# Optimization experiments

Hardware: AMD Instinct MI355X
Metric: run time of the kernel (lower is better)

## Reference

```python
import jax, jax.numpy as jnp
import numpy as np

B, S, D, H = 16, 512, 1024, 16
DH = D // H  # 64


def setup_inputs() -> dict:
    key = jax.random.key(0)
    kx, kq, kk, kv = jax.random.split(key, 4)
    stdv = 1.0 / np.sqrt(DH)  # reset_param uses 1/sqrt(t.size(1)) = 1/sqrt(head_dim)
    x = jax.random.normal(kx, (B, S, D), dtype=jnp.float32)
    Wq = jax.random.uniform(kq, (H, D, DH), dtype=jnp.float32, minval=-stdv, maxval=stdv)
    Wk = jax.random.uniform(kk, (H, D, DH), dtype=jnp.float32, minval=-stdv, maxval=stdv)
    Wv = jax.random.uniform(kv, (H, D, DH), dtype=jnp.float32, minval=-stdv, maxval=stdv)
    return {"x": x, "Wq": Wq, "Wk": Wk, "Wv": Wv}


def reference(x, Wq, Wk, Wv):
    # x: [B, S, D]; Wq/Wk/Wv: [H, D, DH] (stacked per-head params)
    q = jnp.einsum('bsd,hde->bhse', x, Wq)  # [B,H,S,DH]
    k = jnp.einsum('bsd,hde->bhse', x, Wk)
    v = jnp.einsum('bsd,hde->bhse', x, Wv)
    # NOTE: original scales by sqrt(input_dim), not sqrt(head_dim)
    scale = 1.0 / jnp.sqrt(jnp.float32(D))
    scores = jnp.einsum('bhse,bhte->bhst', q, k) * scale  # [B,H,S,S]
    attn = jax.nn.softmax(scores, axis=-1)
    out = jnp.einsum('bhst,bhte->bhse', attn, v)  # [B,H,S,DH]
    # concat heads along feature dim (head order matches torch cat over loop)
    return out.transpose(0, 2, 1, 3).reshape(x.shape[0], x.shape[1], D)
```

## Files before the change

kernel.cpp:

```cpp
#include <hip/hip_runtime.h>
#include <math.h>

constexpr int B = 16, S = 512, D = 1024, H = 16, DH = 64;
constexpr int BH = B * H;

typedef short bf16x8 __attribute__((ext_vector_type(8)));
typedef float f32x4  __attribute__((ext_vector_type(4)));

__device__ __forceinline__ unsigned short f2bf(float f) {
    unsigned u = __float_as_uint(f);
    u += 0x7fff + ((u >> 16) & 1);
    return (unsigned short)(u >> 16);
}

__global__ __launch_bounds__(256) void convert_x(
    const float* __restrict__ x, unsigned short* __restrict__ xb)
{
    int i = blockIdx.x * 256 + threadIdx.x;
    float4 v = ((const float4*)x)[i];
    ushort4 o;
    o.x = f2bf(v.x); o.y = f2bf(v.y); o.z = f2bf(v.z); o.w = f2bf(v.w);
    ((ushort4*)xb)[i] = o;
}

__global__ __launch_bounds__(256) void convert_w(
    const float* __restrict__ Wq, const float* __restrict__ Wk,
    const float* __restrict__ Wv, unsigned short* __restrict__ WbT)
{
    __shared__ float tile[64][65];
    const int d0 = blockIdx.x * 64;
    const int h = blockIdx.y, m = blockIdx.z;
    const float* W = ((m == 0) ? Wq : (m == 1) ? Wk : Wv) + (size_t)h * D * DH;
    const int t = threadIdx.x;
    {
        int e = t & 63, dr = t >> 6;
        #pragma unroll
        for (int i = 0; i < 16; ++i) {
            int d = dr * 16 + i;
            tile[d][e] = W[(size_t)(d0 + d) * DH + e];
        }
    }
    __syncthreads();
    {
        int d = t & 63, er = t >> 6;
        unsigned short* out = WbT + (size_t)(m * H + h) * DH * D;
        #pragma unroll
        for (int i = 0; i < 16; ++i) {
            int e = er * 16 + i;
            out[(size_t)e * D + d0 + d] = f2bf(tile[d][e]);
        }
    }
}

__global__ __launch_bounds__(256) void qkv_gemm(
    const unsigned short* __restrict__ xb,
    const unsigned short* __restrict__ WbT,
    unsigned short* __restrict__ qkvb)
{
    __shared__ unsigned short As[128 * 64];
    __shared__ unsigned short Bs[128 * 64];

    const int t = threadIdx.x;
    const int w = t >> 6;
    const int wr = w >> 1, wc = w & 1;
    const int L = t & 63;
    const int lane15 = L & 15;
    const int quad = L >> 4;
    const int lrow8 = L >> 3;
    const int lg = L & 7;

    const int r0 = blockIdx.x * 128;
    const int n0 = blockIdx.y * 128;

    f32x4 acc[4][4] = {};

    for (int k0 = 0; k0 < D; k0 += 64) {
        #pragma unroll
        for (int i = 0; i < 4; ++i) {
            int c = w * 4 + i;
            int r = c * 8 + lrow8;
            int gg = lg ^ (r & 7);
            const unsigned short* gp = xb + (size_t)(r0 + r) * D + k0 + gg * 8;
            __builtin_amdgcn_global_load_lds(
                (const __attribute__((address_space(1))) void*)gp,
                (__attribute__((address_space(3))) void*)(As + c * 512),
                16, 0, 0);
            const unsigned short* gq = WbT + (size_t)(n0 + r) * D + k0 + gg * 8;
            __builtin_amdgcn_global_load_lds(
                (const __attribute__((address_space(1))) void*)gq,
                (__attribute__((address_space(3))) void*)(Bs + c * 512),
                16, 0, 0);
        }
        __syncthreads();

        #pragma unroll
        for (int ks = 0; ks < 2; ++ks) {
            int gk = ks * 4 + quad;
            bf16x8 a[4], bb[4];
            #pragma unroll
            for (int rt = 0; rt < 4; ++rt) {
                int ml = wr * 64 + rt * 16 + lane15;
                a[rt] = *(const bf16x8*)(As + ml * 64 + ((gk ^ (ml & 7)) * 8));
            }
            #pragma unroll
            for (int ct = 0; ct < 4; ++ct) {
                int nl = wc * 64 + ct * 16 + lane15;
                bb[ct] = *(const bf16x8*)(Bs + nl * 64 + ((gk ^ (nl & 7)) * 8));
            }
            #pragma unroll
            for (int rt = 0; rt < 4; ++rt)
                #pragma unroll
                for (int ct = 0; ct < 4; ++ct)
                    acc[rt][ct] = __builtin_amdgcn_mfma_f32_16x16x32_bf16(
                        a[rt], bb[ct], acc[rt][ct], 0, 0, 0);
        }
        __syncthreads();
    }

    const int m  = n0 >> 10;
    const int h  = ((n0 >> 6) + wc) & 15;
    const int bb_ = r0 >> 9;
    const int s0 = (r0 & 511) + wr * 64;

    if (m == 2) {
        unsigned short* outv = qkvb + ((size_t)(2 * BH) + (bb_ * H + h)) * (size_t)(S * DH);
        #pragma unroll
        for (int rt = 0; rt < 4; ++rt) {
            int srow = s0 + rt * 16 + quad * 4;
            #pragma unroll
            for (int ct = 0; ct < 4; ++ct) {
                int e = ct * 16 + lane15;
                ushort4 pk;
                pk.x = f2bf(acc[rt][ct][0]);
                pk.y = f2bf(acc[rt][ct][1]);
                pk.z = f2bf(acc[rt][ct][2]);
                pk.w = f2bf(acc[rt][ct][3]);
                *(ushort4*)(outv + (size_t)e * S + srow) = pk;
            }
        }
    } else {
        const float sc = (m == 0) ? 0.04508422002778011f : 1.0f;
        unsigned short* out = qkvb + ((size_t)m * BH + (bb_ * H + h)) * (size_t)(S * DH);
        #pragma unroll
        for (int rt = 0; rt < 4; ++rt) {
            #pragma unroll
            for (int ct = 0; ct < 4; ++ct) {
                int e = ct * 16 + lane15;
                #pragma unroll
                for (int r = 0; r < 4; ++r) {
                    int srow = s0 + rt * 16 + quad * 4 + r;
                    out[(size_t)srow * DH + e] = f2bf(acc[rt][ct][r] * sc);
                }
            }
        }
    }
}

__global__ __launch_bounds__(256) void attn_mfma(
    const unsigned short* __restrict__ qkvb, float* __restrict__ out)
{
    __shared__ unsigned short Qs[128 * 64];
    __shared__ unsigned short Ks[64 * 64];
    __shared__ unsigned short Vt[64 * 64];

    const int t = threadIdx.x;
    const int w = t >> 6;
    const int L = t & 63;
    const int lane15 = L & 15;
    const int quad = L >> 4;
    const int lrow8 = L >> 3;
    const int lg = L & 7;
    const int qr0 = blockIdx.x * 128;
    const int bh = blockIdx.y;
    const int b = bh >> 4, h = bh & 15;

    const unsigned short* qb = qkvb + (size_t)bh * S * DH;
    const unsigned short* kb = qkvb + (size_t)(BH + bh) * S * DH;
    const unsigned short* vt = qkvb + (size_t)(2 * BH + bh) * S * DH;

    #pragma unroll
    for (int i = 0; i < 4; ++i) {
        int base = w * 32 + i * 8;
        int r = base + lrow8;
        int gg = lg ^ (r & 7);
        const unsigned short* gp = qb + (size_t)(qr0 + r) * DH + gg * 8;
        __builtin_amdgcn_global_load_lds(
            (const __attribute__((address_space(1))) void*)gp,
            (__attribute__((address_space(3))) void*)(Qs + base * 64),
            16, 0, 0);
    }

    f32x4 o[2][4] = {};
    float plsum[2] = {0.f, 0.f};
    bf16x8 qf[2][2];

    for (int kt = 0; kt < S; kt += 64) {
        #pragma unroll
        for (int i = 0; i < 2; ++i) {
            int base = (w * 2 + i) * 8;
            int r = base + lrow8;
            int gr = (r & 32) | ((r & 12) << 1) | ((r & 16) >> 2) | (r & 3);
            int gg = lg ^ (r & 7);
            const unsigned short* gpk = kb + (size_t)(kt + gr) * DH + gg * 8;
            __builtin_amdgcn_global_load_lds(
                (const __attribute__((address_space(1))) void*)gpk,
                (__attribute__((address_space(3))) void*)(Ks + base * 64),
                16, 0, 0);
            const unsigned short* gpv = vt + (size_t)r * S + kt + gg * 8;
            __builtin_amdgcn_global_load_lds(
                (const __attribute__((address_space(1))) void*)gpv,
                (__attribute__((address_space(3))) void*)(Vt + base * 64),
                16, 0, 0);
        }
        __syncthreads();

        if (kt == 0) {
            #pragma unroll
            for (int mt = 0; mt < 2; ++mt)
                #pragma unroll
                for (int ks = 0; ks < 2; ++ks) {
                    int ml = w * 32 + mt * 16 + lane15;
                    int gk = ks * 4 + quad;
                    qf[mt][ks] = *(const bf16x8*)(Qs + ml * 64 + ((gk ^ (lane15 & 7)) * 8));
                }
        }

        f32x4 st[2][4] = {};
        #pragma unroll
        for (int ks = 0; ks < 2; ++ks) {
            int gk = ks * 4 + quad;
            bf16x8 kf[4];
            #pragma unroll
            for (int ct = 0; ct < 4; ++ct) {
                int kr = ct * 16 + lane15;
                kf[ct] = *(const bf16x8*)(Ks + kr * 64 + ((gk ^ (lane15 & 7)) * 8));
            }
            #pragma unroll
            for (int mt = 0; mt < 2; ++mt)
                #pragma unroll
                for (int ct = 0; ct < 4; ++ct)
                    st[mt][ct] = __builtin_amdgcn_mfma_f32_16x16x32_bf16(
                        kf[ct], qf[mt][ks], st[mt][ct], 0, 0, 0);
        }

        bf16x8 pB[2][2];
        #pragma unroll
        for (int mt = 0; mt < 2; ++mt) {
            float rs = 0.f;
            #pragma unroll
            for (int ct = 0; ct < 4; ++ct) {
                float p0 = exp2f(st[mt][ct][0]);
                float p1 = exp2f(st[mt][ct][1]);
                float p2 = exp2f(st[mt][ct][2]);
                float p3 = exp2f(st[mt][ct][3]);
                rs += (p0 + p1) + (p2 + p3);
                int hi = (ct & 1) * 4;
                pB[mt][ct >> 1][hi + 0] = (short)f2bf(p0);
                pB[mt][ct >> 1][hi + 1] = (short)f2bf(p1);
                pB[mt][ct >> 1][hi + 2] = (short)f2bf(p2);
                pB[mt][ct >> 1][hi + 3] = (short)f2bf(p3);
            }
            plsum[mt] += rs;
        }

        #pragma unroll
        for (int ks = 0; ks < 2; ++ks) {
            int gk = ks * 4 + quad;
            bf16x8 vf[4];
            #pragma unroll
            for (int nt = 0; nt < 4; ++nt) {
                int dh = nt * 16 + lane15;
                vf[nt] = *(const bf16x8*)(Vt + dh * 64 + ((gk ^ (lane15 & 7)) * 8));
            }
            #pragma unroll
            for (int mt = 0; mt < 2; ++mt)
                #pragma unroll
                for (int nt = 0; nt < 4; ++nt)
                    o[mt][nt] = __builtin_amdgcn_mfma_f32_16x16x32_bf16(
                        vf[nt], pB[mt][ks], o[mt][nt], 0, 0, 0);
        }
        __syncthreads();
    }

    #pragma unroll
    for (int mt = 0; mt < 2; ++mt) {
        float l = plsum[mt];
        l += __shfl_xor(l, 16, 64);
        l += __shfl_xor(l, 32, 64);
        float inv = 1.0f / l;
        int srow = qr0 + w * 32 + mt * 16 + lane15;
        float* op = out + (size_t)(b * S + srow) * D + h * DH;
        #pragma unroll
        for (int nt = 0; nt < 4; ++nt) {
            float4 v;
            v.x = o[mt][nt][0] * inv;
            v.y = o[mt][nt][1] * inv;
            v.z = o[mt][nt][2] * inv;
            v.w = o[mt][nt][3] * inv;
            *(float4*)(op + nt * 16 + quad * 4) = v;
        }
    }
}

extern "C" void kernel_launch(void* const* d_in, const int* in_sizes, int n_in,
                              void* d_out, int out_size, void* d_ws, size_t ws_size,
                              hipStream_t stream) {
    const float* x  = (const float*)d_in[0];
    const float* Wq = (const float*)d_in[1];
    const float* Wk = (const float*)d_in[2];
    const float* Wv = (const float*)d_in[3];
    float* outp = (float*)d_out;

    unsigned short* qkvb = (unsigned short*)d_ws;
    unsigned short* xb   = (unsigned short*)((char*)d_ws + 50331648);
    unsigned short* WbT  = (unsigned short*)((char*)d_ws + 67108864);

    convert_x<<<dim3((B * S * D / 4) / 256), 256, 0, stream>>>(x, xb);
    convert_w<<<dim3(D / 64, H, 3), 256, 0, stream>>>(Wq, Wk, Wv, WbT);
    qkv_gemm<<<dim3(B * S / 128, 3 * H * DH / 128), 256, 0, stream>>>(xb, WbT, qkvb);
    attn_mfma<<<dim3(S / 128, BH), 256, 0, stream>>>(qkvb, outp);
}
```

Baseline: 194.5 us.

## Merge conversion kernels and vectorize Q/K epilogue stores via swapped MFMA operands

The separate x and weight bf16 conversion kernels are merged into one launch, with the block index choosing the role, to save one kernel launch. In the QKV GEMM, the Q/K tiles swap the MFMA operand order so each lane holds four consecutive head-dim values of one row. The epilogue can then write packed 8-byte stores instead of scalar 2-byte stores. The cost is a duplicated GEMM main loop behind a block-uniform branch, which enlarges the code.

```diff
diff --git a/kernel.cpp b/kernel.cpp
--- a/kernel.cpp
+++ b/kernel.cpp
@@ -13,25 +13,27 @@
     return (unsigned short)(u >> 16);
 }
 
-__global__ __launch_bounds__(256) void convert_x(
-    const float* __restrict__ x, unsigned short* __restrict__ xb)
-{
-    int i = blockIdx.x * 256 + threadIdx.x;
-    float4 v = ((const float4*)x)[i];
-    ushort4 o;
-    o.x = f2bf(v.x); o.y = f2bf(v.y); o.z = f2bf(v.z); o.w = f2bf(v.w);
-    ((ushort4*)xb)[i] = o;
-}
-
-__global__ __launch_bounds__(256) void convert_w(
+__global__ __launch_bounds__(256) void convert_xw(
+    const float* __restrict__ x,
     const float* __restrict__ Wq, const float* __restrict__ Wk,
-    const float* __restrict__ Wv, unsigned short* __restrict__ WbT)
+    const float* __restrict__ Wv,
+    unsigned short* __restrict__ xb, unsigned short* __restrict__ WbT)
 {
     __shared__ float tile[64][65];
-    const int d0 = blockIdx.x * 64;
-    const int h = blockIdx.y, m = blockIdx.z;
+    const int t = threadIdx.x;
+    if (blockIdx.x < 8192) {
+        int i = blockIdx.x * 256 + t;
+        float4 v = ((const float4*)x)[i];
+        ushort4 o;
+        o.x = f2bf(v.x); o.y = f2bf(v.y); o.z = f2bf(v.z); o.w = f2bf(v.w);
+        ((ushort4*)xb)[i] = o;
+        return;
+    }
+    const int idx = blockIdx.x - 8192;
+    const int d0 = (idx & 15) * 64;
+    const int h = (idx >> 4) & 15;
+    const int m = idx >> 8;
     const float* W = ((m == 0) ? Wq : (m == 1) ? Wk : Wv) + (size_t)h * D * DH;
-    const int t = threadIdx.x;
     {
         int e = t & 63, dr = t >> 6;
         #pragma unroll
@@ -71,53 +73,98 @@
 
     const int r0 = blockIdx.x * 128;
     const int n0 = blockIdx.y * 128;
+    const int m  = n0 >> 10;
 
     f32x4 acc[4][4] = {};
 
-    for (int k0 = 0; k0 < D; k0 += 64) {
-        #pragma unroll
-        for (int i = 0; i < 4; ++i) {
-            int c = w * 4 + i;
-            int r = c * 8 + lrow8;
-            int gg = lg ^ (r & 7);
-            const unsigned short* gp = xb + (size_t)(r0 + r) * D + k0 + gg * 8;
-            __builtin_amdgcn_global_load_lds(
-                (const __attribute__((address_space(1))) void*)gp,
-                (__attribute__((address_space(3))) void*)(As + c * 512),
-                16, 0, 0);
-            const unsigned short* gq = WbT + (size_t)(n0 + r) * D + k0 + gg * 8;
-            __builtin_amdgcn_global_load_lds(
-                (const __attribute__((address_space(1))) void*)gq,
-                (__attribute__((address_space(3))) void*)(Bs + c * 512),
-                16, 0, 0);
-        }
-        __syncthreads();
-
-        #pragma unroll
-        for (int ks = 0; ks < 2; ++ks) {
-            int gk = ks * 4 + quad;
-            bf16x8 a[4], bb[4];
-            #pragma unroll
-            for (int rt = 0; rt < 4; ++rt) {
-                int ml = wr * 64 + rt * 16 + lane15;
-                a[rt] = *(const bf16x8*)(As + ml * 64 + ((gk ^ (ml & 7)) * 8));
-            }
-            #pragma unroll
-            for (int ct = 0; ct < 4; ++ct) {
-                int nl = wc * 64 + ct * 16 + lane15;
-                bb[ct] = *(const bf16x8*)(Bs + nl * 64 + ((gk ^ (nl & 7)) * 8));
-            }
-            #pragma unroll
-            for (int rt = 0; rt < 4; ++rt)
-                #pragma unroll
-                for (int ct = 0; ct < 4; ++ct)
-                    acc[rt][ct] = __builtin_amdgcn_mfma_f32_16x16x32_bf16(
-                        a[rt], bb[ct], acc[rt][ct], 0, 0, 0);
-        }
-        __syncthreads();
-    }
-
-    const int m  = n0 >> 10;
+    if (m == 2) {
+        for (int k0 = 0; k0 < D; k0 += 64) {
+            #pragma unroll
+            for (int i = 0; i < 4; ++i) {
+                int c = w * 4 + i;
+                int r = c * 8 + lrow8;
+                int gg = lg ^ (r & 7);
+                const unsigned short* gp = xb + (size_t)(r0 + r) * D + k0 + gg * 8;
+                __builtin_amdgcn_global_load_lds(
+                    (const __attribute__((address_space(1))) void*)gp,
+                    (__attribute__((address_space(3))) void*)(As + c * 512),
+                    16, 0, 0);
+                const unsigned short* gq = WbT + (size_t)(n0 + r) * D + k0 + gg * 8;
+                __builtin_amdgcn_global_load_lds(
+                    (const __attribute__((address_space(1))) void*)gq,
+                    (__attribute__((address_space(3))) void*)(Bs + c * 512),
+                    16, 0, 0);
+            }
+            __syncthreads();
+
+            #pragma unroll
+            for (int ks = 0; ks < 2; ++ks) {
+                int gk = ks * 4 + quad;
+                bf16x8 a[4], bb[4];
+                #pragma unroll
+                for (int rt = 0; rt < 4; ++rt) {
+                    int ml = wr * 64 + rt * 16 + lane15;
+                    a[rt] = *(const bf16x8*)(As + ml * 64 + ((gk ^ (ml & 7)) * 8));
+                }
+                #pragma unroll
+                for (int ct = 0; ct < 4; ++ct) {
+                    int nl = wc * 64 + ct * 16 + lane15;
+                    bb[ct] = *(const bf16x8*)(Bs + nl * 64 + ((gk ^ (nl & 7)) * 8));
+                }
+                #pragma unroll
+                for (int rt = 0; rt < 4; ++rt)
+                    #pragma unroll
+                    for (int ct = 0; ct < 4; ++ct)
+                        acc[rt][ct] = __builtin_amdgcn_mfma_f32_16x16x32_bf16(
+                            a[rt], bb[ct], acc[rt][ct], 0, 0, 0);
+            }
+            __syncthreads();
+        }
+    } else {
+        for (int k0 = 0; k0 < D; k0 += 64) {
+            #pragma unroll
+            for (int i = 0; i < 4; ++i) {
+                int c = w * 4 + i;
+                int r = c * 8 + lrow8;
+                int gg = lg ^ (r & 7);
+                const unsigned short* gp = xb + (size_t)(r0 + r) * D + k0 + gg * 8;
+                __builtin_amdgcn_global_load_lds(
+                    (const __attribute__((address_space(1))) void*)gp,
+                    (__attribute__((address_space(3))) void*)(As + c * 512),
+                    16, 0, 0);
+                const unsigned short* gq = WbT + (size_t)(n0 + r) * D + k0 + gg * 8;
+                __builtin_amdgcn_global_load_lds(
+                    (const __attribute__((address_space(1))) void*)gq,
+                    (__attribute__((address_space(3))) void*)(Bs + c * 512),
+                    16, 0, 0);
+            }
+            __syncthreads();
+
+            #pragma unroll
+            for (int ks = 0; ks < 2; ++ks) {
+                int gk = ks * 4 + quad;
+                bf16x8 a[4], bb[4];
+                #pragma unroll
+                for (int rt = 0; rt < 4; ++rt) {
+                    int ml = wr * 64 + rt * 16 + lane15;
+                    a[rt] = *(const bf16x8*)(As + ml * 64 + ((gk ^ (ml & 7)) * 8));
+                }
+                #pragma unroll
+                for (int ct = 0; ct < 4; ++ct) {
+                    int nl = wc * 64 + ct * 16 + lane15;
+                    bb[ct] = *(const bf16x8*)(Bs + nl * 64 + ((gk ^ (nl & 7)) * 8));
+                }
+                #pragma unroll
+                for (int rt = 0; rt < 4; ++rt)
+                    #pragma unroll
+                    for (int ct = 0; ct < 4; ++ct)
+                        acc[rt][ct] = __builtin_amdgcn_mfma_f32_16x16x32_bf16(
+                            bb[ct], a[rt], acc[rt][ct], 0, 0, 0);
+            }
+            __syncthreads();
+        }
+    }
+
     const int h  = ((n0 >> 6) + wc) & 15;
     const int bb_ = r0 >> 9;
     const int s0 = (r0 & 511) + wr * 64;
@@ -143,14 +190,16 @@
         unsigned short* out = qkvb + ((size_t)m * BH + (bb_ * H + h)) * (size_t)(S * DH);
         #pragma unroll
         for (int rt = 0; rt < 4; ++rt) {
+            int srow = s0 + rt * 16 + lane15;
             #pragma unroll
             for (int ct = 0; ct < 4; ++ct) {
-                int e = ct * 16 + lane15;
-                #pragma unroll
-                for (int r = 0; r < 4; ++r) {
-                    int srow = s0 + rt * 16 + quad * 4 + r;
-                    out[(size_t)srow * DH + e] = f2bf(acc[rt][ct][r] * sc);
-                }
+                int e0 = ct * 16 + quad * 4;
+                ushort4 pk;
+                pk.x = f2bf(acc[rt][ct][0] * sc);
+                pk.y = f2bf(acc[rt][ct][1] * sc);
+                pk.z = f2bf(acc[rt][ct][2] * sc);
+                pk.w = f2bf(acc[rt][ct][3] * sc);
+                *(ushort4*)(out + (size_t)srow * DH + e0) = pk;
             }
         }
     }
@@ -315,8 +364,7 @@
     unsigned short* xb   = (unsigned short*)((char*)d_ws + 50331648);
     unsigned short* WbT  = (unsigned short*)((char*)d_ws + 67108864);
 
-    convert_x<<<dim3((B * S * D / 4) / 256), 256, 0, stream>>>(x, xb);
-    convert_w<<<dim3(D / 64, H, 3), 256, 0, stream>>>(Wq, Wk, Wv, WbT);
+    convert_xw<<<dim3(8192 + 768), 256, 0, stream>>>(x, Wq, Wk, Wv, xb, WbT);
     qkv_gemm<<<dim3(B * S / 128, 3 * H * DH / 128), 256, 0, stream>>>(xb, WbT, qkvb);
     attn_mfma<<<dim3(S / 128, BH), 256, 0, stream>>>(qkvb, outp);
 }
```

Result: slower. 201.8 us (+3.7%).
